# Optimization experiments

Hardware: AMD Instinct MI355X
Metric: run time of the kernel (lower is better)

Reference implementation:

```python
import jax, jax.numpy as jnp
import numpy as np

B, T, D = 4, 256, 1024
E, DL, TOPK, H = 16, 64, 2, 4


def setup_inputs() -> dict:
    key = jax.random.key(0)
    ks = jax.random.split(key, 12)
    n = lambda k, s: (0.02 * jax.random.normal(k, s)).astype(jnp.float32)
    return dict(
        x=jax.random.normal(ks[0], (B, T, D), dtype=jnp.float32),
        w_down=n(ks[1], (E * DL, D)),
        pos_embed=n(ks[2], (1, E, DL)),
        gp_w=n(ks[3], (DL, D)), gp_b=jnp.zeros((DL,), jnp.float32),
        attn_in_w=n(ks[4], (3 * DL, DL)), attn_in_b=jnp.zeros((3 * DL,), jnp.float32),
        attn_out_w=n(ks[5], (DL, DL)), attn_out_b=jnp.zeros((DL,), jnp.float32),
        ln_w=jnp.ones((DL,), jnp.float32), ln_b=jnp.zeros((DL,), jnp.float32),
        ls_w=n(ks[6], (1, DL)), ls_b=jnp.zeros((1,), jnp.float32),
        g1_w=n(ks[7], (2 * DL, DL)), g1_b=jnp.zeros((2 * DL,), jnp.float32),
        g2_w=n(ks[8], (E, 2 * DL)), g2_b=jnp.zeros((E,), jnp.float32),
        w_up=n(ks[9], (E, DL, D)),
    )


def reference(x, w_down, pos_embed, gp_w, gp_b, attn_in_w, attn_in_b,
              attn_out_w, attn_out_b, ln_w, ln_b, ls_w, ls_b,
              g1_w, g1_b, g2_w, g2_b, w_up):
    Bq, Tq, Dm = x.shape
    N = Bq * Tq
    xf = x.reshape(N, Dm)
    # per-token per-expert low-rank features [N, E, DL]
    ef = (xf @ w_down.T).reshape(N, E, DL)
    # global context per batch element -> [B, DL]
    gctx = x.mean(axis=1) @ gp_w.T + gp_b
    gtok = jnp.repeat(gctx, Tq, axis=0)[:, None, :]  # [N, 1, DL]
    seq = jnp.concatenate([gtok, ef + pos_embed], axis=1)  # [N, E+1, DL]
    # tiny multihead self-attention over E+1 tokens, eval mode (no dropout)
    qkv = seq @ attn_in_w.T + attn_in_b
    q, k, v = jnp.split(qkv, 3, axis=-1)
    hd = DL // H
    sh = lambda t: t.reshape(N, E + 1, H, hd).transpose(0, 2, 1, 3)
    q, k, v = sh(q), sh(k), sh(v)
    scores = jnp.einsum('nhqd,nhkd->nhqk', q, k) / np.float32(np.sqrt(hd))
    attn = jax.nn.softmax(scores, axis=-1)
    ctx = jnp.einsum('nhqk,nhkd->nhqd', attn, v).transpose(0, 2, 1, 3).reshape(N, E + 1, DL)
    attn_out = ctx @ attn_out_w.T + attn_out_b
    h = attn_out + seq
    mu = h.mean(-1, keepdims=True)
    var = h.var(-1, keepdims=True)
    hn = (h - mu) / jnp.sqrt(var + 1e-5) * ln_w + ln_b
    refined = hn[:, 1:, :]  # drop global token -> [N, E, DL]
    local_logits = (refined @ ls_w.T + ls_b)[..., 0]  # [N, E]
    gb = jax.nn.gelu(gctx @ g1_w.T + g1_b, approximate=False) @ g2_w.T + g2_b  # [B, E]
    logits = local_logits + jnp.repeat(gb, Tq, axis=0)
    probs = jax.nn.softmax(logits, axis=-1)
    tw, ti = jax.lax.top_k(probs, TOPK)
    tw = tw / tw.sum(-1, keepdims=True)
    sel = jnp.take_along_axis(ef, ti[..., None], axis=1)  # [N, K, DL]
    act = jax.nn.gelu(sel, approximate=False)
    # gather per-token expert up-projections and batched vec-mat
    eo = jnp.einsum('nkd,nkdm->nkm', act, w_up[ti])  # [N, K, D]
    out = (eo * tw[..., None]).sum(axis=1).reshape(Bq, Tq, Dm)
    mean_prob = probs.mean(axis=0)
    one_hot = jnp.zeros_like(probs).at[jnp.arange(N)[:, None], ti].set(1.0)
    aux_loss = E * jnp.sum(mean_prob * one_hot.mean(axis=0))
    return out, aux_loss
```

## Files before the change

kernel.cpp:

```cpp
#include <hip/hip_runtime.h>
#include <math.h>

#define NB 4
#define TT 256
#define DMODEL 1024
#define NE 16
#define DLQ 64
#define NH 4
#define HD 16
#define SEQL 17
#define NTOK 1024

static constexpr size_t WS_EF    = 0;
static constexpr size_t WS_AH    = 1048576;
static constexpr size_t WS_ACT   = 1048576;
static constexpr size_t WS_AL    = 1572864;
static constexpr size_t WS_WUPT  = 1572864;
static constexpr size_t WS_BH    = 2097152;
static constexpr size_t WS_AIWFH = 2097152;
static constexpr size_t WS_AIWFL = 2103296;
static constexpr size_t WS_AOWFH = 2109440;
static constexpr size_t WS_AOWFL = 2111488;
static constexpr size_t WS_BL    = 2621440;
static constexpr size_t WS_P1    = 3145728;
static constexpr size_t WS_XPART = 4194304;
static constexpr size_t WS_PR    = 4194304;
static constexpr size_t WS_TI    = 4210688;
static constexpr size_t WS_GCTX  = 4227072;
static constexpr size_t WS_GB    = 4227328;

typedef __attribute__((ext_vector_type(8))) short short8;
typedef __attribute__((ext_vector_type(4))) float f32x4;

__device__ __forceinline__ float gelu_exact(float x) {
    return 0.5f * x * (1.0f + erff(x * 0.70710678118654752f));
}

__device__ __forceinline__ unsigned short f2bf(float f) {
    unsigned int u = __float_as_uint(f);
    unsigned int r = (u + 0x7fffu + ((u >> 16) & 1u)) >> 16;
    return (unsigned short)r;
}
__device__ __forceinline__ float bf2f(unsigned short h) {
    return __uint_as_float(((unsigned int)h) << 16);
}

#define DPP_ADD(v, ctrl) { int _m = __builtin_amdgcn_update_dpp(0, __float_as_int(v), ctrl, 0xF, 0xF, true); \
                           v += __int_as_float(_m); }
__device__ __forceinline__ float rsum16(float v) {
    DPP_ADD(v, 0x128);
    DPP_ADD(v, 0x124);
    DPP_ADD(v, 0x122);
    DPP_ADD(v, 0x121);
    return v;
}
__device__ __forceinline__ float rsum64(float v) {
    v = rsum16(v);
    v += __shfl_xor(v, 16);
    v += __shfl_xor(v, 32);
    return v;
}

__global__ __launch_bounds__(256) void k_prep(const float* __restrict__ x,
                                              const float* __restrict__ wdn,
                                              float* __restrict__ ws) {
    int t = blockIdx.x * 256 + threadIdx.x;
    int row = t >> 7;
    int col0 = (t & 127) * 8;
    const float* src = blockIdx.y ? wdn : x;
    unsigned short* hp = (unsigned short*)(ws + (blockIdx.y ? WS_BH : WS_AH));
    unsigned short* lp = (unsigned short*)(ws + (blockIdx.y ? WS_BL : WS_AL));
    float4 v0 = *(const float4*)(src + (size_t)row * DMODEL + col0);
    float4 v1 = *(const float4*)(src + (size_t)row * DMODEL + col0 + 4);
    float vv[8] = {v0.x, v0.y, v0.z, v0.w, v1.x, v1.y, v1.z, v1.w};
    unsigned short h8[8], l8[8];
#pragma unroll
    for (int j = 0; j < 8; ++j) {
        h8[j] = f2bf(vv[j]);
        l8[j] = f2bf(vv[j] - bf2f(h8[j]));
    }
    int nb = row >> 6, kb = col0 >> 6;
    int st = (row & 63) >> 4;
    int ks = (col0 & 63) >> 5;
    int ln = (row & 15) + (((col0 >> 3) & 3) << 4);
    size_t off = (size_t)(nb * 16 + kb) * 4096 + st * 1024 + ks * 512 + ln * 8;
    *(short8*)(hp + off) = *(short8*)h8;
    *(short8*)(lp + off) = *(short8*)l8;
}

__global__ __launch_bounds__(256) void k_batch_partial(const float* __restrict__ x,
                                                       float* __restrict__ ws) {
    int b = blockIdx.x >> 3;
    int g = blockIdx.x & 7;
    int tid = threadIdx.x;
    const float* xp = x + (size_t)b * TT * DMODEL + (size_t)g * 32 * DMODEL + tid * 4;
    float4 acc = {0.f, 0.f, 0.f, 0.f};
#pragma unroll 4
    for (int t = 0; t < 32; ++t) {
        float4 v = *(const float4*)(xp + (size_t)t * DMODEL);
        acc.x += v.x; acc.y += v.y; acc.z += v.z; acc.w += v.w;
    }
    *(float4*)(ws + WS_XPART + (size_t)blockIdx.x * DMODEL + tid * 4) = acc;
}

__global__ __launch_bounds__(256) void k_global_ctx(const float* __restrict__ gp_w,
                                                    const float* __restrict__ gp_b,
                                                    const float* __restrict__ g1_w,
                                                    const float* __restrict__ g1_b,
                                                    const float* __restrict__ g2_w,
                                                    const float* __restrict__ g2_b,
                                                    float* __restrict__ ws) {
    int b = blockIdx.x, tid = threadIdx.x;
    __shared__ float xm[DMODEL];
    __shared__ float gc[DLQ];
    __shared__ float gb1[128];
    float4 a = {0.f, 0.f, 0.f, 0.f};
#pragma unroll
    for (int g = 0; g < 8; ++g) {
        float4 v = *(const float4*)(ws + WS_XPART + (size_t)(b * 8 + g) * DMODEL + tid * 4);
        a.x += v.x; a.y += v.y; a.z += v.z; a.w += v.w;
    }
    const float inv_t = 1.0f / (float)TT;
    xm[tid * 4 + 0] = a.x * inv_t;
    xm[tid * 4 + 1] = a.y * inv_t;
    xm[tid * 4 + 2] = a.z * inv_t;
    xm[tid * 4 + 3] = a.w * inv_t;
    __syncthreads();
    if (tid < DLQ) {
        const float* wr = gp_w + (size_t)tid * DMODEL;
        float s = 0.f;
        for (int j = 0; j < DMODEL; j += 4) {
            float4 w4 = *(const float4*)(wr + j);
            float4 x4 = *(const float4*)&xm[j];
            s += w4.x * x4.x + w4.y * x4.y + w4.z * x4.z + w4.w * x4.w;
        }
        float v = s + gp_b[tid];
        gc[tid] = v;
        ws[WS_GCTX + b * DLQ + tid] = v;
    }
    __syncthreads();
    if (tid < 128) {
        const float* wr = g1_w + (size_t)tid * DLQ;
        float s = 0.f;
        for (int j = 0; j < DLQ; j += 4) {
            float4 w4 = *(const float4*)(wr + j);
            float4 x4 = *(const float4*)&gc[j];
            s += w4.x * x4.x + w4.y * x4.y + w4.z * x4.z + w4.w * x4.w;
        }
        gb1[tid] = gelu_exact(s + g1_b[tid]);
    }
    __syncthreads();
    if (tid < NE) {
        const float* wr = g2_w + (size_t)tid * 128;
        float s = 0.f;
        for (int j = 0; j < 128; ++j) s += wr[j] * gb1[j];
        ws[WS_GB + b * NE + tid] = s + g2_b[tid];
    }
}

__global__ __launch_bounds__(256) void k_ef_mfma(float* __restrict__ ws) {
    __shared__ __attribute__((aligned(16))) unsigned short smem[16384];
    const unsigned short* AhP = (const unsigned short*)(ws + WS_AH);
    const unsigned short* AlP = (const unsigned short*)(ws + WS_AL);
    const unsigned short* BhP = (const unsigned short*)(ws + WS_BH);
    const unsigned short* BlP = (const unsigned short*)(ws + WS_BL);
    int tid = threadIdx.x;
    int mb = blockIdx.x;
    int nb = blockIdx.y;
    int kz = blockIdx.z;
    int w = tid >> 6, l = tid & 63;
    int wn = (w >> 1) * 32, wm = (w & 1) * 32;
    int stA = wn >> 4, stB = wm >> 4;
    f32x4 acc00 = {0.f, 0.f, 0.f, 0.f}, acc01 = acc00, acc10 = acc00, acc11 = acc00;

    for (int it = 0; it < 8; ++it) {
        int kb = kz * 8 + it;
        const char* srcs[4] = {
            (const char*)(AhP + (size_t)(nb * 16 + kb) * 4096),
            (const char*)(AlP + (size_t)(nb * 16 + kb) * 4096),
            (const char*)(BhP + (size_t)(mb * 16 + kb) * 4096),
            (const char*)(BlP + (size_t)(mb * 16 + kb) * 4096)};
#pragma unroll
        for (int p = 0; p < 4; ++p) {
#pragma unroll
            for (int h = 0; h < 2; ++h) {
                __builtin_amdgcn_global_load_lds(
                    (const __attribute__((address_space(1))) void*)(srcs[p] + h * 4096 + tid * 16),
                    (__attribute__((address_space(3))) void*)((char*)smem + p * 8192 + h * 4096 + tid * 16),
                    16, 0, 0);
            }
        }
        __syncthreads();
        const unsigned short* Ah = smem;
        const unsigned short* Al = smem + 4096;
        const unsigned short* Bh = smem + 8192;
        const unsigned short* Bl = smem + 12288;
#pragma unroll
        for (int ks = 0; ks < 2; ++ks) {
            short8 ah0 = *(const short8*)(Ah + (stA + 0) * 1024 + ks * 512 + l * 8);
            short8 ah1 = *(const short8*)(Ah + (stA + 1) * 1024 + ks * 512 + l * 8);
            short8 al0 = *(const short8*)(Al + (stA + 0) * 1024 + ks * 512 + l * 8);
            short8 al1 = *(const short8*)(Al + (stA + 1) * 1024 + ks * 512 + l * 8);
            short8 bh0 = *(const short8*)(Bh + (stB + 0) * 1024 + ks * 512 + l * 8);
            short8 bh1 = *(const short8*)(Bh + (stB + 1) * 1024 + ks * 512 + l * 8);
            short8 bl0 = *(const short8*)(Bl + (stB + 0) * 1024 + ks * 512 + l * 8);
            short8 bl1 = *(const short8*)(Bl + (stB + 1) * 1024 + ks * 512 + l * 8);
            acc00 = __builtin_amdgcn_mfma_f32_16x16x32_bf16(ah0, bh0, acc00, 0, 0, 0);
            acc00 = __builtin_amdgcn_mfma_f32_16x16x32_bf16(al0, bh0, acc00, 0, 0, 0);
            acc00 = __builtin_amdgcn_mfma_f32_16x16x32_bf16(ah0, bl0, acc00, 0, 0, 0);
            acc01 = __builtin_amdgcn_mfma_f32_16x16x32_bf16(ah0, bh1, acc01, 0, 0, 0);
            acc01 = __builtin_amdgcn_mfma_f32_16x16x32_bf16(al0, bh1, acc01, 0, 0, 0);
            acc01 = __builtin_amdgcn_mfma_f32_16x16x32_bf16(ah0, bl1, acc01, 0, 0, 0);
            acc10 = __builtin_amdgcn_mfma_f32_16x16x32_bf16(ah1, bh0, acc10, 0, 0, 0);
            acc10 = __builtin_amdgcn_mfma_f32_16x16x32_bf16(al1, bh0, acc10, 0, 0, 0);
            acc10 = __builtin_amdgcn_mfma_f32_16x16x32_bf16(ah1, bl0, acc10, 0, 0, 0);
            acc11 = __builtin_amdgcn_mfma_f32_16x16x32_bf16(ah1, bh1, acc11, 0, 0, 0);
            acc11 = __builtin_amdgcn_mfma_f32_16x16x32_bf16(al1, bh1, acc11, 0, 0, 0);
            acc11 = __builtin_amdgcn_mfma_f32_16x16x32_bf16(ah1, bl1, acc11, 0, 0, 0);
        }
        __syncthreads();
    }
    int cr = (l >> 4) * 4, cc = l & 15;
    int n0 = nb * 64, m0 = mb * 64;
    float* P = ws + (kz == 0 ? WS_EF : WS_P1);
#pragma unroll
    for (int r = 0; r < 4; ++r) {
        P[(size_t)(n0 + wn + cr + r) * DMODEL + (m0 + wm + cc)]           = acc00[r];
        P[(size_t)(n0 + wn + cr + r) * DMODEL + (m0 + wm + 16 + cc)]      = acc01[r];
        P[(size_t)(n0 + wn + 16 + cr + r) * DMODEL + (m0 + wm + cc)]      = acc10[r];
        P[(size_t)(n0 + wn + 16 + cr + r) * DMODEL + (m0 + wm + 16 + cc)] = acc11[r];
    }
}

__global__ __launch_bounds__(256) void k_prep_wup(const float* __restrict__ w_up,
                                                  const float* __restrict__ aiw,
                                                  const float* __restrict__ aow,
                                                  float* __restrict__ ws) {
    int e = blockIdx.x, ct = blockIdx.y, tid = threadIdx.x;
    __shared__ float tile[64][65];
#pragma unroll
    for (int jj = 0; jj < 16; ++jj) {
        int j = jj * 4 + (tid >> 6);
        tile[j][tid & 63] = w_up[((size_t)e * DLQ + j) * DMODEL + ct * 64 + (tid & 63)];
    }
    __syncthreads();
    int c = tid >> 2, j0 = (tid & 3) * 16;
    unsigned short* dst = (unsigned short*)(ws + WS_WUPT) +
                          (size_t)e * 65536 + (size_t)(ct * 64 + c) * 64 + j0;
#pragma unroll
    for (int q = 0; q < 4; ++q) {
        ushort4 o;
        o.x = f2bf(tile[j0 + q * 4 + 0][c]);
        o.y = f2bf(tile[j0 + q * 4 + 1][c]);
        o.z = f2bf(tile[j0 + q * 4 + 2][c]);
        o.w = f2bf(tile[j0 + q * 4 + 3][c]);
        *(ushort4*)(dst + q * 4) = o;
    }
    if (e == 0 && ct == 1) {
        unsigned short* fh = (unsigned short*)(ws + WS_AIWFH);
        unsigned short* fl = (unsigned short*)(ws + WS_AIWFL);
        for (int idx = tid; idx < 12 * 2 * 64; idx += 256) {
            int nt = idx >> 7, kf = (idx >> 6) & 1, l = idx & 63;
            int row = nt * 16 + (l & 15);
            int k = kf * 32 + ((l >> 4) << 3);
            const float* src = aiw + (size_t)row * DLQ + k;
            unsigned short h8[8], l8[8];
#pragma unroll
            for (int j = 0; j < 8; ++j) {
                h8[j] = f2bf(src[j]);
                l8[j] = f2bf(src[j] - bf2f(h8[j]));
            }
            size_t off = (size_t)(nt * 2 + kf) * 512 + l * 8;
            *(short8*)(fh + off) = *(short8*)h8;
            *(short8*)(fl + off) = *(short8*)l8;
        }
    }
    if (e == 0 && ct == 2) {
        unsigned short* gh = (unsigned short*)(ws + WS_AOWFH);
        unsigned short* gl = (unsigned short*)(ws + WS_AOWFL);
        for (int idx = tid; idx < 4 * 2 * 64; idx += 256) {
            int nt = idx >> 7, kf = (idx >> 6) & 1, l = idx & 63;
            int row = nt * 16 + (l & 15);
            int k = kf * 32 + ((l >> 4) << 3);
            const float* src = aow + (size_t)row * DLQ + k;
            unsigned short h8[8], l8[8];
#pragma unroll
            for (int j = 0; j < 8; ++j) {
                h8[j] = f2bf(src[j]);
                l8[j] = f2bf(src[j] - bf2f(h8[j]));
            }
            size_t off = (size_t)(nt * 2 + kf) * 512 + l * 8;
            *(short8*)(gh + off) = *(short8*)h8;
            *(short8*)(gl + off) = *(short8*)l8;
        }
    }
}

__global__ __launch_bounds__(128) void k_attn2(const float* __restrict__ pos_embed,
                                               const float* __restrict__ attn_in_b,
                                               const float* __restrict__ attn_out_b,
                                               const float* __restrict__ ln_w,
                                               const float* __restrict__ ln_b,
                                               const float* __restrict__ ls_w,
                                               const float* __restrict__ ls_b,
                                               float* __restrict__ ws) {
    int n = blockIdx.x;
    int w = threadIdx.x >> 6;
    int l = threadIdx.x & 63;
    int b = n >> 8;

    __shared__ float qkv[SEQL * 200];
    __shared__ __attribute__((aligned(16))) char ubuf[8192];
    __shared__ __attribute__((aligned(16))) unsigned short ctxH[1024];
    __shared__ __attribute__((aligned(16))) unsigned short ctxL[1024];
    __shared__ float lgv_sh[NE];
    unsigned short* sH = (unsigned short*)ubuf;
    unsigned short* sL = (unsigned short*)(ubuf + 4096);
    float* ao = (float*)ubuf;

    float seqc[SEQL];
    {
        const float* efp0 = ws + WS_EF + (size_t)n * DMODEL;
        const float* efp1 = ws + WS_P1 + (size_t)n * DMODEL;
        float gcv = ws[WS_GCTX + b * DLQ + l];
#pragma unroll
        for (int i = 0; i < SEQL; ++i) {
            float s = (i == 0) ? gcv
                               : efp0[(i - 1) * DLQ + l] + efp1[(i - 1) * DLQ + l] +
                                 pos_embed[(i - 1) * DLQ + l];
            seqc[i] = s;
            int lo_r = w * 9, hi_r = w * 9 + 8;
            if (i >= lo_r && i <= hi_r && i < SEQL) {
                unsigned short hs = f2bf(s);
                unsigned short lsv = f2bf(s - bf2f(hs));
                int mt = i >> 4;
                int ls = (i & 15) + (((l >> 3) & 3) << 4);
                int kf = l >> 5;
                int j = l & 7;
                size_t off = (size_t)(mt * 2 + kf) * 512 + ls * 8 + j;
                sH[off] = hs;
                sL[off] = lsv;
            }
        }
    }
    __syncthreads();

    {
        const unsigned short* fh = (const unsigned short*)(ws + WS_AIWFH);
        const unsigned short* fl = (const unsigned short*)(ws + WS_AIWFL);
        f32x4 acc[6][2];
#pragma unroll
        for (int t = 0; t < 6; ++t)
#pragma unroll
            for (int m = 0; m < 2; ++m) acc[t][m] = (f32x4){0.f, 0.f, 0.f, 0.f};
#pragma unroll
        for (int kf = 0; kf < 2; ++kf) {
            short8 ah0 = *(const short8*)(sH + (0 * 2 + kf) * 512 + l * 8);
            short8 ah1 = *(const short8*)(sH + (1 * 2 + kf) * 512 + l * 8);
            short8 al0 = *(const short8*)(sL + (0 * 2 + kf) * 512 + l * 8);
            short8 al1 = *(const short8*)(sL + (1 * 2 + kf) * 512 + l * 8);
#pragma unroll
            for (int t = 0; t < 6; ++t) {
                int nt = w * 6 + t;
                short8 bh = *(const short8*)(fh + (size_t)(nt * 2 + kf) * 512 + l * 8);
                short8 bl = *(const short8*)(fl + (size_t)(nt * 2 + kf) * 512 + l * 8);
                acc[t][0] = __builtin_amdgcn_mfma_f32_16x16x32_bf16(ah0, bh, acc[t][0], 0, 0, 0);
                acc[t][0] = __builtin_amdgcn_mfma_f32_16x16x32_bf16(al0, bh, acc[t][0], 0, 0, 0);
                acc[t][0] = __builtin_amdgcn_mfma_f32_16x16x32_bf16(ah0, bl, acc[t][0], 0, 0, 0);
                acc[t][1] = __builtin_amdgcn_mfma_f32_16x16x32_bf16(ah1, bh, acc[t][1], 0, 0, 0);
                acc[t][1] = __builtin_amdgcn_mfma_f32_16x16x32_bf16(al1, bh, acc[t][1], 0, 0, 0);
                acc[t][1] = __builtin_amdgcn_mfma_f32_16x16x32_bf16(ah1, bl, acc[t][1], 0, 0, 0);
            }
        }
#pragma unroll
        for (int t = 0; t < 6; ++t) {
            int col = (w * 6 + t) * 16 + (l & 15);
            float bias = attn_in_b[col];
#pragma unroll
            for (int r = 0; r < 4; ++r) {
                int row = (l >> 4) * 4 + r;
                qkv[row * 200 + col] = acc[t][0][r] + bias;
            }
            if ((l >> 4) == 0) qkv[16 * 200 + col] = acc[t][1][0] + bias;
        }
    }
    __syncthreads();

    {
        int g = l >> 4;
        float kc[SEQL], vc[SEQL];
#pragma unroll
        for (int j = 0; j < SEQL; ++j) {
            kc[j] = qkv[j * 200 + 64 + g * 16 + (l & 15)];
            vc[j] = qkv[j * 200 + 128 + l];
        }
        for (int i = w * 8 + 1; i <= w * 8 + 8; ++i) {
            float qi = qkv[i * 200 + g * 16 + (l & 15)];
            float sj[SEQL];
#pragma unroll
            for (int j = 0; j < SEQL; ++j) {
                sj[j] = rsum16(qi * kc[j]) * 0.25f;
            }
            float m = sj[0];
#pragma unroll
            for (int j = 1; j < SEQL; ++j) m = fmaxf(m, sj[j]);
            float ssum = 0.f;
#pragma unroll
            for (int j = 0; j < SEQL; ++j) { sj[j] = __expf(sj[j] - m); ssum += sj[j]; }
            float inv = 1.f / ssum;
            float c = 0.f;
#pragma unroll
            for (int j = 0; j < SEQL; ++j) c += sj[j] * vc[j];
            c *= inv;
            unsigned short ch = f2bf(c);
            unsigned short cl = f2bf(c - bf2f(ch));
            int ls = ((i - 1) & 15) + (((l >> 3) & 3) << 4);
            int kf = l >> 5;
            int j2 = l & 7;
            size_t off = (size_t)kf * 512 + ls * 8 + j2;
            ctxH[off] = ch;
            ctxL[off] = cl;
        }
    }
    __syncthreads();

    {
        const unsigned short* gh = (const unsigned short*)(ws + WS_AOWFH);
        const unsigned short* gl = (const unsigned short*)(ws + WS_AOWFL);
        f32x4 acc[2];
        acc[0] = (f32x4){0.f, 0.f, 0.f, 0.f};
        acc[1] = acc[0];
#pragma unroll
        for (int kf = 0; kf < 2; ++kf) {
            short8 ah = *(const short8*)(ctxH + kf * 512 + l * 8);
            short8 al = *(const short8*)(ctxL + kf * 512 + l * 8);
#pragma unroll
            for (int t = 0; t < 2; ++t) {
                int nt = w * 2 + t;
                short8 bh = *(const short8*)(gh + (size_t)(nt * 2 + kf) * 512 + l * 8);
                short8 bl = *(const short8*)(gl + (size_t)(nt * 2 + kf) * 512 + l * 8);
                acc[t] = __builtin_amdgcn_mfma_f32_16x16x32_bf16(ah, bh, acc[t], 0, 0, 0);
                acc[t] = __builtin_amdgcn_mfma_f32_16x16x32_bf16(al, bh, acc[t], 0, 0, 0);
                acc[t] = __builtin_amdgcn_mfma_f32_16x16x32_bf16(ah, bl, acc[t], 0, 0, 0);
            }
        }
        __syncthreads();
#pragma unroll
        for (int t = 0; t < 2; ++t) {
            int col = (w * 2 + t) * 16 + (l & 15);
            float bias = attn_out_b[col];
#pragma unroll
            for (int r = 0; r < 4; ++r) {
                int row = (l >> 4) * 4 + r;
                ao[row * 72 + col] = acc[t][r] + bias;
            }
        }
    }
    __syncthreads();

    float rs[SEQL];
#pragma unroll
    for (int i = 1; i < SEQL; ++i) rs[i] = seqc[i] + ao[(i - 1) * 72 + l];

    float c1 = ln_w[l] * ls_w[l];
    float c1sum = rsum64(c1);
    float c0sum = rsum64(ln_b[l] * ls_w[l]);
    float lsb0 = ls_b[0];
#pragma unroll
    for (int ee = 0; ee < 8; ++ee) {
        int e = w * 8 + ee;
        float x = rs[e + 1];
        float s1 = rsum64(x);
        float s2 = rsum64(x * x);
        float s3 = rsum64(x * c1);
        float mu = s1 * (1.0f / DLQ);
        float var = s2 * (1.0f / DLQ) - mu * mu;
        float rstd = rsqrtf(var + 1e-5f);
        float lgv = rstd * (s3 - mu * c1sum) + c0sum + lsb0 + ws[WS_GB + b * NE + e];
        if (l == 0) lgv_sh[e] = lgv;
    }
    __syncthreads();

    if (w == 0) {
        float p[NE];
        float lgv[NE];
#pragma unroll
        for (int e = 0; e < NE; ++e) lgv[e] = lgv_sh[e];
        float m = lgv[0];
#pragma unroll
        for (int e = 1; e < NE; ++e) m = fmaxf(m, lgv[e]);
        float ssum = 0.f;
#pragma unroll
        for (int e = 0; e < NE; ++e) { p[e] = __expf(lgv[e] - m); ssum += p[e]; }
        float inv = 1.f / ssum;
#pragma unroll
        for (int e = 0; e < NE; ++e) p[e] *= inv;
        int t0 = 0; float b0 = p[0];
#pragma unroll
        for (int e = 1; e < NE; ++e) if (p[e] > b0) { b0 = p[e]; t0 = e; }
        int t1 = -1; float b1 = -1.f;
#pragma unroll
        for (int e = 0; e < NE; ++e) if (e != t0 && p[e] > b1) { b1 = p[e]; t1 = e; }

        float sw = b0 + b1;
        float tw0 = b0 / sw, tw1 = b1 / sw;
        unsigned short* actp = (unsigned short*)(ws + WS_ACT);
        float efv0 = ws[WS_EF + (size_t)n * DMODEL + t0 * DLQ + l] +
                     ws[WS_P1 + (size_t)n * DMODEL + t0 * DLQ + l];
        float efv1 = ws[WS_EF + (size_t)n * DMODEL + t1 * DLQ + l] +
                     ws[WS_P1 + (size_t)n * DMODEL + t1 * DLQ + l];
        actp[(size_t)(n * 2 + 0) * 64 + l] = f2bf(gelu_exact(efv0) * tw0);
        actp[(size_t)(n * 2 + 1) * 64 + l] = f2bf(gelu_exact(efv1) * tw1);
        if (l == 0) {
#pragma unroll
            for (int e = 0; e < NE; ++e) ws[WS_PR + (size_t)n * NE + e] = p[e];
            ((int*)(ws + WS_TI))[n] = t0 | (t1 << 8);
        }
    }
}

__global__ __launch_bounds__(256) void k_moe_gemm(float* __restrict__ ws,
                                                  float* __restrict__ out) {
    int e = blockIdx.x, ct = blockIdx.y;
    int tid = threadIdx.x;
    int wv = tid >> 6, l = tid & 63;
    __shared__ int lst[2048];
    __shared__ int lcnt;
    if (tid == 0) lcnt = 0;
    __syncthreads();
    {
        const int* tip = (const int*)(ws + WS_TI);
#pragma unroll
        for (int c = 0; c < 4; ++c) {
            int tok = wv * 256 + c * 64 + l;
            int pk = tip[tok];
            bool m1 = ((pk >> 8) & 0xff) == e;
            bool m = ((pk & 0xff) == e) || m1;
            unsigned long long mask = __ballot(m);
            int base = 0;
            if (l == 0 && mask) base = atomicAdd(&lcnt, __popcll(mask));
            base = __shfl(base, 0);
            if (m) {
                int pos = base + __popcll(mask & ((1ull << l) - 1ull));
                lst[pos] = tok * 2 + (m1 ? 1 : 0);
            }
        }
    }
    __syncthreads();
    int cnt = lcnt;
    if (cnt == 0) return;

    const unsigned short* wupt = (const unsigned short*)(ws + WS_WUPT) + (size_t)e * 65536;
    const unsigned short* actp = (const unsigned short*)(ws + WS_ACT);
    int col = ct * 64 + wv * 16 + (l & 15);
    int kb = (l >> 4) * 8;
    short8 bf0 = *(const short8*)(wupt + (size_t)col * 64 + kb);
    short8 bf1 = *(const short8*)(wupt + (size_t)col * 64 + 32 + kb);
    int cr = (l >> 4) * 4;

    for (int mt = 0; mt < cnt; mt += 16) {
        int row = mt + (l & 15);
        short8 a0 = {0, 0, 0, 0, 0, 0, 0, 0};
        short8 a1 = {0, 0, 0, 0, 0, 0, 0, 0};
        if (row < cnt) {
            int pk = lst[row];
            a0 = *(const short8*)(actp + (size_t)pk * 64 + kb);
            a1 = *(const short8*)(actp + (size_t)pk * 64 + 32 + kb);
        }
        f32x4 acc = {0.f, 0.f, 0.f, 0.f};
        acc = __builtin_amdgcn_mfma_f32_16x16x32_bf16(a0, bf0, acc, 0, 0, 0);
        acc = __builtin_amdgcn_mfma_f32_16x16x32_bf16(a1, bf1, acc, 0, 0, 0);
#pragma unroll
        for (int r = 0; r < 4; ++r) {
            int rr = mt + cr + r;
            if (rr < cnt) {
                int pk = lst[rr];
                atomicAdd(&out[(size_t)(pk >> 1) * DMODEL + col], acc[r]);
            }
        }
    }
}

__global__ __launch_bounds__(256) void k_aux(const float* __restrict__ ws, float* __restrict__ out) {
    int tid = threadIdx.x;
    __shared__ float wsum[4][NE];
    __shared__ int hist[NE];
    if (tid < NE) hist[tid] = 0;
    __syncthreads();
    {
        const int* tip = (const int*)(ws + WS_TI);
#pragma unroll
        for (int c = 0; c < 4; ++c) {
            int pk = tip[tid * 4 + c];
            atomicAdd(&hist[pk & 0xff], 1);
            atomicAdd(&hist[(pk >> 8) & 0xff], 1);
        }
    }
    float p[NE];
#pragma unroll
    for (int e = 0; e < NE; ++e) p[e] = 0.f;
    const float* pr = ws + WS_PR + (size_t)tid * 64;
#pragma unroll
    for (int r = 0; r < 4; ++r)
#pragma unroll
        for (int q = 0; q < 4; ++q) {
            float4 v = *(const float4*)(pr + r * 16 + q * 4);
            p[q * 4 + 0] += v.x; p[q * 4 + 1] += v.y;
            p[q * 4 + 2] += v.z; p[q * 4 + 3] += v.w;
        }
#pragma unroll
    for (int e = 0; e < NE; ++e) p[e] = rsum64(p[e]);
    int w = tid >> 6, l = tid & 63;
    if (l == 0) {
#pragma unroll
        for (int e = 0; e < NE; ++e) wsum[w][e] = p[e];
    }
    __syncthreads();
    if (tid == 0) {
        float s = 0.f;
#pragma unroll
        for (int e = 0; e < NE; ++e) {
            float sp = wsum[0][e] + wsum[1][e] + wsum[2][e] + wsum[3][e];
            s += sp * (float)hist[e];
        }
        out[(size_t)NTOK * DMODEL] = (float)NE * s / ((float)NTOK * (float)NTOK);
    }
}

extern "C" void kernel_launch(void* const* d_in, const int* in_sizes, int n_in,
                              void* d_out, int out_size, void* d_ws, size_t ws_size,
                              hipStream_t stream) {
    const float* x          = (const float*)d_in[0];
    const float* w_down     = (const float*)d_in[1];
    const float* pos_embed  = (const float*)d_in[2];
    const float* gp_w       = (const float*)d_in[3];
    const float* gp_b       = (const float*)d_in[4];
    const float* attn_in_w  = (const float*)d_in[5];
    const float* attn_in_b  = (const float*)d_in[6];
    const float* attn_out_w = (const float*)d_in[7];
    const float* attn_out_b = (const float*)d_in[8];
    const float* ln_w       = (const float*)d_in[9];
    const float* ln_b       = (const float*)d_in[10];
    const float* ls_w       = (const float*)d_in[11];
    const float* ls_b       = (const float*)d_in[12];
    const float* g1_w       = (const float*)d_in[13];
    const float* g1_b       = (const float*)d_in[14];
    const float* g2_w       = (const float*)d_in[15];
    const float* g2_b       = (const float*)d_in[16];
    const float* w_up       = (const float*)d_in[17];
    float* ws  = (float*)d_ws;
    float* out = (float*)d_out;

    hipMemsetAsync(out, 0, (size_t)out_size * sizeof(float), stream);
    k_prep<<<dim3(512, 2), 256, 0, stream>>>(x, w_down, ws);
    k_batch_partial<<<32, 256, 0, stream>>>(x, ws);
    k_global_ctx<<<NB, 256, 0, stream>>>(gp_w, gp_b, g1_w, g1_b, g2_w, g2_b, ws);
    k_ef_mfma<<<dim3(16, 16, 2), 256, 0, stream>>>(ws);
    k_prep_wup<<<dim3(16, 16), 256, 0, stream>>>(w_up, attn_in_w, attn_out_w, ws);
    k_attn2<<<NTOK, 128, 0, stream>>>(pos_embed, attn_in_b, attn_out_b,
                                      ln_w, ln_b, ls_w, ls_b, ws);
    k_moe_gemm<<<dim3(NE, 16), 256, 0, stream>>>(ws, out);
    k_aux<<<1, 256, 0, stream>>>(ws, out);
}
```

Baseline: 184.2 us.

## Fold weight prep, drop split-K in ef GEMM, merge aux into MoE kernel

Moves the w_up transpose and attention-weight bf16 split into the k_prep launch as extra blocks. It also removes split-K from the ef MFMA GEMM, so each block runs the full K loop and writes ef directly, which drops the P1 partial buffer and the extra adds in the attention kernel. The aux-loss kernel becomes an extra block column of k_moe_gemm. Together this cuts two launches and some memory traffic, at the cost of half as many blocks in the ef GEMM and some relocated workspace offsets.

```diff
diff --git a/kernel.cpp b/kernel.cpp
--- a/kernel.cpp
+++ b/kernel.cpp
@@ -15,14 +15,13 @@
 static constexpr size_t WS_AH    = 1048576;
 static constexpr size_t WS_ACT   = 1048576;
 static constexpr size_t WS_AL    = 1572864;
-static constexpr size_t WS_WUPT  = 1572864;
 static constexpr size_t WS_BH    = 2097152;
-static constexpr size_t WS_AIWFH = 2097152;
-static constexpr size_t WS_AIWFL = 2103296;
-static constexpr size_t WS_AOWFH = 2109440;
-static constexpr size_t WS_AOWFL = 2111488;
 static constexpr size_t WS_BL    = 2621440;
-static constexpr size_t WS_P1    = 3145728;
+static constexpr size_t WS_WUPT  = 3145728;
+static constexpr size_t WS_AIWFH = 3670016;
+static constexpr size_t WS_AIWFL = 3676160;
+static constexpr size_t WS_AOWFH = 3682304;
+static constexpr size_t WS_AOWFL = 3684352;
 static constexpr size_t WS_XPART = 4194304;
 static constexpr size_t WS_PR    = 4194304;
 static constexpr size_t WS_TI    = 4210688;
@@ -63,29 +62,93 @@
 
 __global__ __launch_bounds__(256) void k_prep(const float* __restrict__ x,
                                               const float* __restrict__ wdn,
+                                              const float* __restrict__ w_up,
+                                              const float* __restrict__ aiw,
+                                              const float* __restrict__ aow,
                                               float* __restrict__ ws) {
-    int t = blockIdx.x * 256 + threadIdx.x;
-    int row = t >> 7;
-    int col0 = (t & 127) * 8;
-    const float* src = blockIdx.y ? wdn : x;
-    unsigned short* hp = (unsigned short*)(ws + (blockIdx.y ? WS_BH : WS_AH));
-    unsigned short* lp = (unsigned short*)(ws + (blockIdx.y ? WS_BL : WS_AL));
-    float4 v0 = *(const float4*)(src + (size_t)row * DMODEL + col0);
-    float4 v1 = *(const float4*)(src + (size_t)row * DMODEL + col0 + 4);
-    float vv[8] = {v0.x, v0.y, v0.z, v0.w, v1.x, v1.y, v1.z, v1.w};
-    unsigned short h8[8], l8[8];
-#pragma unroll
-    for (int j = 0; j < 8; ++j) {
-        h8[j] = f2bf(vv[j]);
-        l8[j] = f2bf(vv[j] - bf2f(h8[j]));
-    }
-    int nb = row >> 6, kb = col0 >> 6;
-    int st = (row & 63) >> 4;
-    int ks = (col0 & 63) >> 5;
-    int ln = (row & 15) + (((col0 >> 3) & 3) << 4);
-    size_t off = (size_t)(nb * 16 + kb) * 4096 + st * 1024 + ks * 512 + ln * 8;
-    *(short8*)(hp + off) = *(short8*)h8;
-    *(short8*)(lp + off) = *(short8*)l8;
+    __shared__ float tile[64][65];
+    int bi = blockIdx.x;
+    int tid = threadIdx.x;
+    if (bi < 1024) {
+        int which = bi >> 9;
+        int t = (bi & 511) * 256 + tid;
+        int row = t >> 7;
+        int col0 = (t & 127) * 8;
+        const float* src = which ? wdn : x;
+        unsigned short* hp = (unsigned short*)(ws + (which ? WS_BH : WS_AH));
+        unsigned short* lp = (unsigned short*)(ws + (which ? WS_BL : WS_AL));
+        float4 v0 = *(const float4*)(src + (size_t)row * DMODEL + col0);
+        float4 v1 = *(const float4*)(src + (size_t)row * DMODEL + col0 + 4);
+        float vv[8] = {v0.x, v0.y, v0.z, v0.w, v1.x, v1.y, v1.z, v1.w};
+        unsigned short h8[8], l8[8];
+#pragma unroll
+        for (int j = 0; j < 8; ++j) {
+            h8[j] = f2bf(vv[j]);
+            l8[j] = f2bf(vv[j] - bf2f(h8[j]));
+        }
+        int nb = row >> 6, kb = col0 >> 6;
+        int st = (row & 63) >> 4;
+        int ks = (col0 & 63) >> 5;
+        int ln = (row & 15) + (((col0 >> 3) & 3) << 4);
+        size_t off = (size_t)(nb * 16 + kb) * 4096 + st * 1024 + ks * 512 + ln * 8;
+        *(short8*)(hp + off) = *(short8*)h8;
+        *(short8*)(lp + off) = *(short8*)l8;
+    } else if (bi < 1280) {
+        int e = (bi - 1024) >> 4, ct = (bi - 1024) & 15;
+#pragma unroll
+        for (int jj = 0; jj < 16; ++jj) {
+            int j = jj * 4 + (tid >> 6);
+            tile[j][tid & 63] = w_up[((size_t)e * DLQ + j) * DMODEL + ct * 64 + (tid & 63)];
+        }
+        __syncthreads();
+        int c = tid >> 2, j0 = (tid & 3) * 16;
+        unsigned short* dst = (unsigned short*)(ws + WS_WUPT) +
+                              (size_t)e * 65536 + (size_t)(ct * 64 + c) * 64 + j0;
+#pragma unroll
+        for (int q = 0; q < 4; ++q) {
+            ushort4 o;
+            o.x = f2bf(tile[j0 + q * 4 + 0][c]);
+            o.y = f2bf(tile[j0 + q * 4 + 1][c]);
+            o.z = f2bf(tile[j0 + q * 4 + 2][c]);
+            o.w = f2bf(tile[j0 + q * 4 + 3][c]);
+            *(ushort4*)(dst + q * 4) = o;
+        }
+    } else {
+        unsigned short* fh = (unsigned short*)(ws + WS_AIWFH);
+        unsigned short* fl = (unsigned short*)(ws + WS_AIWFL);
+        for (int idx = tid; idx < 12 * 2 * 64; idx += 256) {
+            int nt = idx >> 7, kf = (idx >> 6) & 1, l = idx & 63;
+            int row = nt * 16 + (l & 15);
+            int k = kf * 32 + ((l >> 4) << 3);
+            const float* src = aiw + (size_t)row * DLQ + k;
+            unsigned short h8[8], l8[8];
+#pragma unroll
+            for (int j = 0; j < 8; ++j) {
+                h8[j] = f2bf(src[j]);
+                l8[j] = f2bf(src[j] - bf2f(h8[j]));
+            }
+            size_t off = (size_t)(nt * 2 + kf) * 512 + l * 8;
+            *(short8*)(fh + off) = *(short8*)h8;
+            *(short8*)(fl + off) = *(short8*)l8;
+        }
+        unsigned short* gh = (unsigned short*)(ws + WS_AOWFH);
+        unsigned short* gl = (unsigned short*)(ws + WS_AOWFL);
+        for (int idx = tid; idx < 4 * 2 * 64; idx += 256) {
+            int nt = idx >> 7, kf = (idx >> 6) & 1, l = idx & 63;
+            int row = nt * 16 + (l & 15);
+            int k = kf * 32 + ((l >> 4) << 3);
+            const float* src = aow + (size_t)row * DLQ + k;
+            unsigned short h8[8], l8[8];
+#pragma unroll
+            for (int j = 0; j < 8; ++j) {
+                h8[j] = f2bf(src[j]);
+                l8[j] = f2bf(src[j] - bf2f(h8[j]));
+            }
+            size_t off = (size_t)(nt * 2 + kf) * 512 + l * 8;
+            *(short8*)(gh + off) = *(short8*)h8;
+            *(short8*)(gl + off) = *(short8*)l8;
+        }
+    }
 }
 
 __global__ __launch_bounds__(256) void k_batch_partial(const float* __restrict__ x,
@@ -167,14 +230,12 @@
     int tid = threadIdx.x;
     int mb = blockIdx.x;
     int nb = blockIdx.y;
-    int kz = blockIdx.z;
     int w = tid >> 6, l = tid & 63;
     int wn = (w >> 1) * 32, wm = (w & 1) * 32;
     int stA = wn >> 4, stB = wm >> 4;
     f32x4 acc00 = {0.f, 0.f, 0.f, 0.f}, acc01 = acc00, acc10 = acc00, acc11 = acc00;
 
-    for (int it = 0; it < 8; ++it) {
-        int kb = kz * 8 + it;
+    for (int kb = 0; kb < 16; ++kb) {
         const char* srcs[4] = {
             (const char*)(AhP + (size_t)(nb * 16 + kb) * 4096),
             (const char*)(AlP + (size_t)(nb * 16 + kb) * 4096),
@@ -222,77 +283,13 @@
     }
     int cr = (l >> 4) * 4, cc = l & 15;
     int n0 = nb * 64, m0 = mb * 64;
-    float* P = ws + (kz == 0 ? WS_EF : WS_P1);
+    float* P = ws + WS_EF;
 #pragma unroll
     for (int r = 0; r < 4; ++r) {
         P[(size_t)(n0 + wn + cr + r) * DMODEL + (m0 + wm + cc)]           = acc00[r];
         P[(size_t)(n0 + wn + cr + r) * DMODEL + (m0 + wm + 16 + cc)]      = acc01[r];
         P[(size_t)(n0 + wn + 16 + cr + r) * DMODEL + (m0 + wm + cc)]      = acc10[r];
         P[(size_t)(n0 + wn + 16 + cr + r) * DMODEL + (m0 + wm + 16 + cc)] = acc11[r];
-    }
-}
-
-__global__ __launch_bounds__(256) void k_prep_wup(const float* __restrict__ w_up,
-                                                  const float* __restrict__ aiw,
-                                                  const float* __restrict__ aow,
-                                                  float* __restrict__ ws) {
-    int e = blockIdx.x, ct = blockIdx.y, tid = threadIdx.x;
-    __shared__ float tile[64][65];
-#pragma unroll
-    for (int jj = 0; jj < 16; ++jj) {
-        int j = jj * 4 + (tid >> 6);
-        tile[j][tid & 63] = w_up[((size_t)e * DLQ + j) * DMODEL + ct * 64 + (tid & 63)];
-    }
-    __syncthreads();
-    int c = tid >> 2, j0 = (tid & 3) * 16;
-    unsigned short* dst = (unsigned short*)(ws + WS_WUPT) +
-                          (size_t)e * 65536 + (size_t)(ct * 64 + c) * 64 + j0;
-#pragma unroll
-    for (int q = 0; q < 4; ++q) {
-        ushort4 o;
-        o.x = f2bf(tile[j0 + q * 4 + 0][c]);
-        o.y = f2bf(tile[j0 + q * 4 + 1][c]);
-        o.z = f2bf(tile[j0 + q * 4 + 2][c]);
-        o.w = f2bf(tile[j0 + q * 4 + 3][c]);
-        *(ushort4*)(dst + q * 4) = o;
-    }
-    if (e == 0 && ct == 1) {
-        unsigned short* fh = (unsigned short*)(ws + WS_AIWFH);
-        unsigned short* fl = (unsigned short*)(ws + WS_AIWFL);
-        for (int idx = tid; idx < 12 * 2 * 64; idx += 256) {
-            int nt = idx >> 7, kf = (idx >> 6) & 1, l = idx & 63;
-            int row = nt * 16 + (l & 15);
-            int k = kf * 32 + ((l >> 4) << 3);
-            const float* src = aiw + (size_t)row * DLQ + k;
-            unsigned short h8[8], l8[8];
-#pragma unroll
-            for (int j = 0; j < 8; ++j) {
-                h8[j] = f2bf(src[j]);
-                l8[j] = f2bf(src[j] - bf2f(h8[j]));
-            }
-            size_t off = (size_t)(nt * 2 + kf) * 512 + l * 8;
-            *(short8*)(fh + off) = *(short8*)h8;
-            *(short8*)(fl + off) = *(short8*)l8;
-        }
-    }
-    if (e == 0 && ct == 2) {
-        unsigned short* gh = (unsigned short*)(ws + WS_AOWFH);
-        unsigned short* gl = (unsigned short*)(ws + WS_AOWFL);
-        for (int idx = tid; idx < 4 * 2 * 64; idx += 256) {
-            int nt = idx >> 7, kf = (idx >> 6) & 1, l = idx & 63;
-            int row = nt * 16 + (l & 15);
-            int k = kf * 32 + ((l >> 4) << 3);
-            const float* src = aow + (size_t)row * DLQ + k;
-            unsigned short h8[8], l8[8];
-#pragma unroll
-            for (int j = 0; j < 8; ++j) {
-                h8[j] = f2bf(src[j]);
-                l8[j] = f2bf(src[j] - bf2f(h8[j]));
-            }
-            size_t off = (size_t)(nt * 2 + kf) * 512 + l * 8;
-            *(short8*)(gh + off) = *(short8*)h8;
-            *(short8*)(gl + off) = *(short8*)l8;
-        }
     }
 }
 
@@ -320,14 +317,11 @@
 
     float seqc[SEQL];
     {
-        const float* efp0 = ws + WS_EF + (size_t)n * DMODEL;
-        const float* efp1 = ws + WS_P1 + (size_t)n * DMODEL;
+        const float* efp = ws + WS_EF + (size_t)n * DMODEL;
         float gcv = ws[WS_GCTX + b * DLQ + l];
 #pragma unroll
         for (int i = 0; i < SEQL; ++i) {
-            float s = (i == 0) ? gcv
-                               : efp0[(i - 1) * DLQ + l] + efp1[(i - 1) * DLQ + l] +
-                                 pos_embed[(i - 1) * DLQ + l];
+            float s = (i == 0) ? gcv : efp[(i - 1) * DLQ + l] + pos_embed[(i - 1) * DLQ + l];
             seqc[i] = s;
             int lo_r = w * 9, hi_r = w * 9 + 8;
             if (i >= lo_r && i <= hi_r && i < SEQL) {
@@ -505,10 +499,8 @@
         float sw = b0 + b1;
         float tw0 = b0 / sw, tw1 = b1 / sw;
         unsigned short* actp = (unsigned short*)(ws + WS_ACT);
-        float efv0 = ws[WS_EF + (size_t)n * DMODEL + t0 * DLQ + l] +
-                     ws[WS_P1 + (size_t)n * DMODEL + t0 * DLQ + l];
-        float efv1 = ws[WS_EF + (size_t)n * DMODEL + t1 * DLQ + l] +
-                     ws[WS_P1 + (size_t)n * DMODEL + t1 * DLQ + l];
+        float efv0 = ws[WS_EF + (size_t)n * DMODEL + t0 * DLQ + l];
+        float efv1 = ws[WS_EF + (size_t)n * DMODEL + t1 * DLQ + l];
         actp[(size_t)(n * 2 + 0) * 64 + l] = f2bf(gelu_exact(efv0) * tw0);
         actp[(size_t)(n * 2 + 1) * 64 + l] = f2bf(gelu_exact(efv1) * tw1);
         if (l == 0) {
@@ -521,11 +513,58 @@
 
 __global__ __launch_bounds__(256) void k_moe_gemm(float* __restrict__ ws,
                                                   float* __restrict__ out) {
-    int e = blockIdx.x, ct = blockIdx.y;
+    __shared__ int lst[2048];
+    __shared__ int lcnt;
+    __shared__ float wsum[4][NE];
+    __shared__ int hist[NE];
     int tid = threadIdx.x;
     int wv = tid >> 6, l = tid & 63;
-    __shared__ int lst[2048];
-    __shared__ int lcnt;
+
+    if (blockIdx.x == NE) {
+        if (blockIdx.y != 0) return;
+        if (tid < NE) hist[tid] = 0;
+        __syncthreads();
+        {
+            const int* tip = (const int*)(ws + WS_TI);
+#pragma unroll
+            for (int c = 0; c < 4; ++c) {
+                int pk = tip[tid * 4 + c];
+                atomicAdd(&hist[pk & 0xff], 1);
+                atomicAdd(&hist[(pk >> 8) & 0xff], 1);
+            }
+        }
+        float p[NE];
+#pragma unroll
+        for (int e = 0; e < NE; ++e) p[e] = 0.f;
+        const float* pr = ws + WS_PR + (size_t)tid * 64;
+#pragma unroll
+        for (int r = 0; r < 4; ++r)
+#pragma unroll
+            for (int q = 0; q < 4; ++q) {
+                float4 v = *(const float4*)(pr + r * 16 + q * 4);
+                p[q * 4 + 0] += v.x; p[q * 4 + 1] += v.y;
+                p[q * 4 + 2] += v.z; p[q * 4 + 3] += v.w;
+            }
+#pragma unroll
+        for (int e = 0; e < NE; ++e) p[e] = rsum64(p[e]);
+        if (l == 0) {
+#pragma unroll
+            for (int e = 0; e < NE; ++e) wsum[wv][e] = p[e];
+        }
+        __syncthreads();
+        if (tid == 0) {
+            float s = 0.f;
+#pragma unroll
+            for (int e = 0; e < NE; ++e) {
+                float sp = wsum[0][e] + wsum[1][e] + wsum[2][e] + wsum[3][e];
+                s += sp * (float)hist[e];
+            }
+            out[(size_t)NTOK * DMODEL] = (float)NE * s / ((float)NTOK * (float)NTOK);
+        }
+        return;
+    }
+
+    int e = blockIdx.x, ct = blockIdx.y;
     if (tid == 0) lcnt = 0;
     __syncthreads();
     {
@@ -578,52 +617,6 @@
                 atomicAdd(&out[(size_t)(pk >> 1) * DMODEL + col], acc[r]);
             }
         }
-    }
-}
-
-__global__ __launch_bounds__(256) void k_aux(const float* __restrict__ ws, float* __restrict__ out) {
-    int tid = threadIdx.x;
-    __shared__ float wsum[4][NE];
-    __shared__ int hist[NE];
-    if (tid < NE) hist[tid] = 0;
-    __syncthreads();
-    {
-        const int* tip = (const int*)(ws + WS_TI);
-#pragma unroll
-        for (int c = 0; c < 4; ++c) {
-            int pk = tip[tid * 4 + c];
-            atomicAdd(&hist[pk & 0xff], 1);
-            atomicAdd(&hist[(pk >> 8) & 0xff], 1);
-        }
-    }
-    float p[NE];
-#pragma unroll
-    for (int e = 0; e < NE; ++e) p[e] = 0.f;
-    const float* pr = ws + WS_PR + (size_t)tid * 64;
-#pragma unroll
-    for (int r = 0; r < 4; ++r)
-#pragma unroll
-        for (int q = 0; q < 4; ++q) {
-            float4 v = *(const float4*)(pr + r * 16 + q * 4);
-            p[q * 4 + 0] += v.x; p[q * 4 + 1] += v.y;
-            p[q * 4 + 2] += v.z; p[q * 4 + 3] += v.w;
-        }
-#pragma unroll
-    for (int e = 0; e < NE; ++e) p[e] = rsum64(p[e]);
-    int w = tid >> 6, l = tid & 63;
-    if (l == 0) {
-#pragma unroll
-        for (int e = 0; e < NE; ++e) wsum[w][e] = p[e];
-    }
-    __syncthreads();
-    if (tid == 0) {
-        float s = 0.f;
-#pragma unroll
-        for (int e = 0; e < NE; ++e) {
-            float sp = wsum[0][e] + wsum[1][e] + wsum[2][e] + wsum[3][e];
-            s += sp * (float)hist[e];
-        }
-        out[(size_t)NTOK * DMODEL] = (float)NE * s / ((float)NTOK * (float)NTOK);
     }
 }
 
@@ -652,13 +645,11 @@
     float* out = (float*)d_out;
 
     hipMemsetAsync(out, 0, (size_t)out_size * sizeof(float), stream);
-    k_prep<<<dim3(512, 2), 256, 0, stream>>>(x, w_down, ws);
+    k_prep<<<1281, 256, 0, stream>>>(x, w_down, w_up, attn_in_w, attn_out_w, ws);
     k_batch_partial<<<32, 256, 0, stream>>>(x, ws);
     k_global_ctx<<<NB, 256, 0, stream>>>(gp_w, gp_b, g1_w, g1_b, g2_w, g2_b, ws);
-    k_ef_mfma<<<dim3(16, 16, 2), 256, 0, stream>>>(ws);
-    k_prep_wup<<<dim3(16, 16), 256, 0, stream>>>(w_up, attn_in_w, attn_out_w, ws);
+    k_ef_mfma<<<dim3(16, 16), 256, 0, stream>>>(ws);
     k_attn2<<<NTOK, 128, 0, stream>>>(pos_embed, attn_in_b, attn_out_b,
                                       ln_w, ln_b, ls_w, ls_b, ws);
-    k_moe_gemm<<<dim3(NE, 16), 256, 0, stream>>>(ws, out);
-    k_aux<<<1, 256, 0, stream>>>(ws, out);
-}
+    k_moe_gemm<<<dim3(NE + 1, 16), 256, 0, stream>>>(ws, out);
+}
```

Measured after the change: 186.5 us. No clear change (+1.2%).
